# Optimization experiments

Measured on AMD Instinct MI355X. Metric: run time of the kernel, lower is better.

The kernel has to match this reference:

```python
import jax, jax.numpy as jnp
import numpy as np

B, M, D = 512, 96, 512
H = 8            # num_heads
DH = D // H      # head dim
NC = 3           # num_clusters
BETA = 5
MEM = 1024       # memory_size
EPS = 1e-8


def _l2norm(x, axis=-1):
    # torch F.cosine_similarity clamps each norm at eps=1e-8
    n = jnp.linalg.norm(x, axis=axis, keepdims=True)
    return x / jnp.maximum(n, EPS)


def _dynamic_clustering(sims):
    # sims: (B, M). Sort descending, split into NC equal groups,
    # per-group mean and (unbiased) std. (dynamic_clustering is not
    # defined in the source repo; this is the assumed implementation.)
    s = -jnp.sort(-sims, axis=1)               # descending
    g = s.reshape(B, NC, M // NC)
    means = g.mean(axis=-1)                    # (B, NC)
    stds = jnp.std(g, axis=-1, ddof=1)         # (B, NC)
    return means, stds


def setup_inputs() -> dict:
    key = jax.random.key(0)
    ks = jax.random.split(key, 6)
    vis_global = jax.random.normal(ks[0], (B, D), dtype=jnp.float32)
    text_features = jax.random.normal(ks[1], (B, M, D), dtype=jnp.float32)
    scale = 1.0 / np.sqrt(D)
    in_proj_w = jax.random.normal(ks[2], (3 * D, D), dtype=jnp.float32) * scale
    in_proj_b = jnp.zeros((3 * D,), dtype=jnp.float32)
    out_proj_w = jax.random.normal(ks[3], (D, D), dtype=jnp.float32) * scale
    out_proj_b = jnp.zeros((D,), dtype=jnp.float32)
    text_memory = jax.random.normal(ks[4], (MEM, D), dtype=jnp.float32)
    tau_p_log = jnp.log(jnp.asarray(0.1, dtype=jnp.float32))
    tau_n_log = jnp.log(jnp.asarray(0.05, dtype=jnp.float32))
    return dict(vis_global=vis_global, text_features=text_features,
                in_proj_w=in_proj_w, in_proj_b=in_proj_b,
                out_proj_w=out_proj_w, out_proj_b=out_proj_b,
                text_memory=text_memory, tau_p_log=tau_p_log, tau_n_log=tau_n_log)


def reference(vis_global, text_features, in_proj_w, in_proj_b,
              out_proj_w, out_proj_b, text_memory, tau_p_log, tau_n_log):
    # --- dynamic clustering over visual-text cosine sims ---
    sims = jnp.einsum('bd,bmd->bm', _l2norm(vis_global), _l2norm(text_features))
    means, stds = _dynamic_clustering(sims)
    cluster_scores = means / (stds + 1e-6)     # (B, NC)

    # --- MultiheadAttention: 1-token query, M-token key/value ---
    wq, wk, wv = in_proj_w[:D], in_proj_w[D:2 * D], in_proj_w[2 * D:]
    bq, bk, bv = in_proj_b[:D], in_proj_b[D:2 * D], in_proj_b[2 * D:]
    q = (vis_global @ wq.T + bq).reshape(B, H, DH)              # (B,H,DH)
    k = (text_features @ wk.T + bk).reshape(B, M, H, DH)        # (B,M,H,DH)
    v = (text_features @ wv.T + bv).reshape(B, M, H, DH)
    attn = jax.nn.softmax(jnp.einsum('bhd,bmhd->bhm', q, k) / np.sqrt(DH), axis=-1)
    ctx = jnp.einsum('bhm,bmhd->bhd', attn, v).reshape(B, D)
    corrected = ctx @ out_proj_w.T + out_proj_b                 # (B, D)

    tau_p = jnp.exp(tau_p_log)
    tau_n = jnp.exp(tau_n_log)
    pos_sim = jnp.sum(_l2norm(vis_global) * _l2norm(corrected), axis=-1)  # (B,)

    # memory-bank scatter (ptr starts at 0) + negatives, all detached
    corr_sg = jax.lax.stop_gradient(corrected)
    mem = text_memory.at[0:B].set(corr_sg)
    all_negs = jnp.concatenate([jnp.roll(corr_sg, 1, axis=0), mem], axis=0)  # (B+MEM, D)

    neg_sims = _l2norm(vis_global) @ _l2norm(all_negs).T        # (B, B+MEM)
    hard_negs, _ = jax.lax.top_k(neg_sims, BETA)                # (B, BETA)

    pos_term = jnp.exp(pos_sim / tau_p)
    neg_terms = jnp.exp(hard_negs / tau_n).sum(axis=1)
    loss = -jnp.mean(jnp.log(pos_term / (pos_term + neg_terms + 1e-8)))
    return loss, corrected, cluster_scores
```

## Files before the change

### kernel.cpp

```cpp
#include <hip/hip_runtime.h>
#include <math.h>

typedef unsigned short u16;
typedef unsigned int u32;
typedef __attribute__((ext_vector_type(8))) short short8;
typedef __attribute__((ext_vector_type(4))) float f32x4;

#define EPS 1e-8f

__device__ inline float bf2f(u16 u) {
    union { u32 i; float f; } v; v.i = ((u32)u) << 16; return v.f;
}
__device__ inline u16 f2bf(float f) {
    union { float f; u32 u; } v; v.f = f;
    u32 r = v.u + 0x7fffu + ((v.u >> 16) & 1u);
    return (u16)(r >> 16);
}
__device__ inline u32 pack2(float a, float b) {
    return (u32)f2bf(a) | ((u32)f2bf(b) << 16);
}
__device__ inline float wave_sum(float v) {
    for (int off = 32; off; off >>= 1) v += __shfl_xor(v, off, 64);
    return v;
}

__global__ __launch_bounds__(256) void prep(const float* __restrict__ vis,
                                            const float* __restrict__ ipw,
                                            const float* __restrict__ opw,
                                            float* __restrict__ vis_n,
                                            u16* __restrict__ vis_nb,
                                            u16* __restrict__ vis_b,
                                            u16* __restrict__ wqb,
                                            u16* __restrict__ wvb,
                                            u16* __restrict__ wob,
                                            float* __restrict__ loss0)
{
    int bid = blockIdx.x;
    if (bid >= 128) {
        int i = ((bid - 128) * 256 + threadIdx.x) * 4;
        const float* src; u16* dst; int j;
        if (i < 262144)      { j = i;          src = ipw + j;          dst = wqb + j; }
        else if (i < 524288) { j = i - 262144; src = ipw + 524288 + j; dst = wvb + j; }
        else                 { j = i - 524288; src = opw + j;          dst = wob + j; }
        float4 v = *(const float4*)src;
        uint2 pk; pk.x = pack2(v.x, v.y); pk.y = pack2(v.z, v.w);
        *(uint2*)dst = pk;
        return;
    }
    if (bid == 0 && threadIdx.x == 0) loss0[0] = 0.0f;
    int wave = threadIdx.x >> 6, lane = threadIdx.x & 63;
    int b = bid * 4 + wave;
    const float* row = vis + b * 512 + lane * 8;
    float4 x0 = *(const float4*)row;
    float4 x1 = *(const float4*)(row + 4);
    uint4 rk;
    rk.x = pack2(x0.x, x0.y); rk.y = pack2(x0.z, x0.w);
    rk.z = pack2(x1.x, x1.y); rk.w = pack2(x1.z, x1.w);
    *(uint4*)(vis_b + b*512 + lane*8) = rk;
    float ss = x0.x*x0.x + x0.y*x0.y + x0.z*x0.z + x0.w*x0.w
             + x1.x*x1.x + x1.y*x1.y + x1.z*x1.z + x1.w*x1.w;
    ss = wave_sum(ss);
    float inv = 1.0f / fmaxf(sqrtf(ss), EPS);
    float4 y0, y1;
    y0.x = x0.x*inv; y0.y = x0.y*inv; y0.z = x0.z*inv; y0.w = x0.w*inv;
    y1.x = x1.x*inv; y1.y = x1.y*inv; y1.z = x1.z*inv; y1.w = x1.w*inv;
    *(float4*)(vis_n + b*512 + lane*8)     = y0;
    *(float4*)(vis_n + b*512 + lane*8 + 4) = y1;
    uint4 pk;
    pk.x = pack2(y0.x, y0.y); pk.y = pack2(y0.z, y0.w);
    pk.z = pack2(y1.x, y1.y); pk.w = pack2(y1.z, y1.w);
    *(uint4*)(vis_nb + b*512 + lane*8) = pk;
}

__global__ __launch_bounds__(256) void gemm64(const u16* __restrict__ A, int lda,
                                              const u16* __restrict__ B,
                                              const float* __restrict__ bias,
                                              float* __restrict__ Cf, int ldc)
{
    __shared__ __align__(16) u16 As[64 * 64];
    __shared__ __align__(16) u16 Bs[64 * 64];
    const int t = threadIdx.x, lane = t & 63, w = t >> 6;
    const int m0 = blockIdx.x * 64, n0 = blockIdx.y * 64;
    const int wm = (w >> 1) * 32, wn = (w & 1) * 32;
    const int l16 = lane & 15, quad = lane >> 4;
    const int srow = t >> 3, scol = (t & 7) * 8;

    f32x4 acc[2][2];
    for (int i = 0; i < 2; i++)
        for (int j = 0; j < 2; j++)
            for (int e = 0; e < 4; e++) acc[i][j][e] = 0.f;

    for (int ko = 0; ko < 512; ko += 64) {
        __syncthreads();
        #pragma unroll
        for (int i = 0; i < 2; i++) {
            int row = i * 32 + srow;
            *(uint4*)&As[row * 64 + scol] = *(const uint4*)&A[(size_t)(m0 + row) * lda + ko + scol];
            *(uint4*)&Bs[row * 64 + scol] = *(const uint4*)&B[(size_t)(n0 + row) * 512 + ko + scol];
        }
        __syncthreads();
        #pragma unroll
        for (int ks = 0; ks < 2; ks++) {
            short8 af[2], bfr[2];
            #pragma unroll
            for (int i = 0; i < 2; i++)
                af[i] = *(const short8*)&As[(wm + i * 16 + l16) * 64 + ks * 32 + quad * 8];
            #pragma unroll
            for (int j = 0; j < 2; j++)
                bfr[j] = *(const short8*)&Bs[(wn + j * 16 + l16) * 64 + ks * 32 + quad * 8];
            #pragma unroll
            for (int i = 0; i < 2; i++)
                #pragma unroll
                for (int j = 0; j < 2; j++)
                    acc[i][j] = __builtin_amdgcn_mfma_f32_16x16x32_bf16(af[i], bfr[j], acc[i][j], 0, 0, 0);
        }
    }
    for (int i = 0; i < 2; i++) {
        int row = m0 + wm + i * 16 + quad * 4;
        for (int j = 0; j < 2; j++) {
            int col = n0 + wn + j * 16 + l16;
            float bv = bias ? bias[col] : 0.f;
            for (int r = 0; r < 4; r++)
                Cf[(size_t)(row + r) * ldc + col] = acc[i][j][r] + bv;
        }
    }
}

__global__ __launch_bounds__(256) void gemm_head(const u16* __restrict__ u_allb,
                                                 const u16* __restrict__ wvb,
                                                 const float* __restrict__ bv,
                                                 u16* __restrict__ ctxb)
{
    const int h = blockIdx.y;
    const u16* A = u_allb + h * 512;
    const u16* B = wvb + (size_t)h * 64 * 512;
    __shared__ __align__(16) u16 As[64 * 64];
    __shared__ __align__(16) u16 Bs[64 * 64];
    const int t = threadIdx.x, lane = t & 63, w = t >> 6;
    const int m0 = blockIdx.x * 64;
    const int wm = (w >> 1) * 32, wn = (w & 1) * 32;
    const int l16 = lane & 15, quad = lane >> 4;
    const int srow = t >> 3, scol = (t & 7) * 8;

    f32x4 acc[2][2];
    for (int i = 0; i < 2; i++)
        for (int j = 0; j < 2; j++)
            for (int e = 0; e < 4; e++) acc[i][j][e] = 0.f;

    for (int ko = 0; ko < 512; ko += 64) {
        __syncthreads();
        #pragma unroll
        for (int i = 0; i < 2; i++) {
            int row = i * 32 + srow;
            *(uint4*)&As[row * 64 + scol] = *(const uint4*)&A[(size_t)(m0 + row) * 4096 + ko + scol];
            *(uint4*)&Bs[row * 64 + scol] = *(const uint4*)&B[(size_t)row * 512 + ko + scol];
        }
        __syncthreads();
        #pragma unroll
        for (int ks = 0; ks < 2; ks++) {
            short8 af[2], bfr[2];
            #pragma unroll
            for (int i = 0; i < 2; i++)
                af[i] = *(const short8*)&As[(wm + i * 16 + l16) * 64 + ks * 32 + quad * 8];
            #pragma unroll
            for (int j = 0; j < 2; j++)
                bfr[j] = *(const short8*)&Bs[(wn + j * 16 + l16) * 64 + ks * 32 + quad * 8];
            #pragma unroll
            for (int i = 0; i < 2; i++)
                #pragma unroll
                for (int j = 0; j < 2; j++)
                    acc[i][j] = __builtin_amdgcn_mfma_f32_16x16x32_bf16(af[i], bfr[j], acc[i][j], 0, 0, 0);
        }
    }
    for (int i = 0; i < 2; i++) {
        int row = m0 + wm + i * 16 + quad * 4;
        for (int j = 0; j < 2; j++) {
            int col = wn + j * 16 + l16;
            float bb = bv[h * 64 + col];
            for (int r = 0; r < 4; r++)
                ctxb[(size_t)(row + r) * 512 + h * 64 + col] = f2bf(acc[i][j][r] + bb);
        }
    }
}

__global__ __launch_bounds__(256) void qk_proj(const float* __restrict__ q,
                                               const float* __restrict__ wk,
                                               float* __restrict__ qk_all)
{
    int bg = blockIdx.x, h = blockIdx.y;
    int t = threadIdx.x;
    int j = blockIdx.z * 256 + t;
    __shared__ float q8[8][64];
    {
        int r = t >> 5;
        int d0 = (t & 31) * 2;
        const float* qp = q + (bg * 8 + r) * 512 + h * 64 + d0;
        q8[r][d0] = qp[0]; q8[r][d0 + 1] = qp[1];
    }
    __syncthreads();
    float acc[8] = {0, 0, 0, 0, 0, 0, 0, 0};
    const float* wrow = wk + (size_t)(h * 64) * 512 + j;
    #pragma unroll 4
    for (int d = 0; d < 64; d++) {
        float ww = wrow[(size_t)d * 512];
        #pragma unroll
        for (int r = 0; r < 8; r++) acc[r] += q8[r][d] * ww;
    }
    #pragma unroll
    for (int r = 0; r < 8; r++)
        qk_all[((size_t)(bg * 8 + r) * 8 + h) * 512 + j] = acc[r];
}

__global__ __launch_bounds__(1024) void fused_attn(const float* __restrict__ tf,
                                                   const float* __restrict__ vis_n,
                                                   const float* __restrict__ qk_all,
                                                   u16* __restrict__ u_allb,
                                                   float* __restrict__ out_cs)
{
    __shared__ __align__(16) u16 Xs[96 * 520];
    __shared__ __align__(16) u16 Qs[16 * 520];
    __shared__ __align__(16) u16 Ps[16 * 104];
    __shared__ float Sc[16 * 100];
    __shared__ float sm_[96], srt[96], linv[8];

    const int b = blockIdx.x;
    const int t = threadIdx.x, w = t >> 6, lane = t & 63;
    const int l16 = lane & 15, quad = lane >> 4;

    const float4* v4 = (const float4*)(vis_n + b * 512 + lane * 8);
    float4 va = v4[0], vb = v4[1];

    if (w < 8) {
        const float4* q4 = (const float4*)(qk_all + ((size_t)b * 8 + w) * 512 + lane * 8);
        float4 a = q4[0], c = q4[1];
        uint4 pk;
        pk.x = pack2(a.x, a.y); pk.y = pack2(a.z, a.w);
        pk.z = pack2(c.x, c.y); pk.w = pack2(c.z, c.w);
        *(uint4*)&Qs[w * 520 + lane * 8] = pk;
    }

    #pragma unroll
    for (int i = 0; i < 3; i++) {
        int m0r = w + i * 32;
        int m1r = m0r + 16;
        const float4* x4a = (const float4*)(tf + ((size_t)b * 96 + m0r) * 512 + lane * 8);
        const float4* x4b = (const float4*)(tf + ((size_t)b * 96 + m1r) * 512 + lane * 8);
        float4 a0 = x4a[0], c0 = x4a[1];
        float4 a1 = x4b[0], c1 = x4b[1];
        float ss0 = a0.x*a0.x + a0.y*a0.y + a0.z*a0.z + a0.w*a0.w
                  + c0.x*c0.x + c0.y*c0.y + c0.z*c0.z + c0.w*c0.w;
        float dt0 = a0.x*va.x + a0.y*va.y + a0.z*va.z + a0.w*va.w
                  + c0.x*vb.x + c0.y*vb.y + c0.z*vb.z + c0.w*vb.w;
        float ss1 = a1.x*a1.x + a1.y*a1.y + a1.z*a1.z + a1.w*a1.w
                  + c1.x*c1.x + c1.y*c1.y + c1.z*c1.z + c1.w*c1.w;
        float dt1 = a1.x*va.x + a1.y*va.y + a1.z*va.z + a1.w*va.w
                  + c1.x*vb.x + c1.y*vb.y + c1.z*vb.z + c1.w*vb.w;
        #pragma unroll
        for (int off = 32; off; off >>= 1) {
            ss0 += __shfl_xor(ss0, off, 64);
            dt0 += __shfl_xor(dt0, off, 64);
            ss1 += __shfl_xor(ss1, off, 64);
            dt1 += __shfl_xor(dt1, off, 64);
        }
        if (lane == 0) {
            sm_[m0r] = dt0 / fmaxf(sqrtf(ss0), EPS);
            sm_[m1r] = dt1 / fmaxf(sqrtf(ss1), EPS);
        }
        uint4 pk0, pk1;
        pk0.x = pack2(a0.x, a0.y); pk0.y = pack2(a0.z, a0.w);
        pk0.z = pack2(c0.x, c0.y); pk0.w = pack2(c0.z, c0.w);
        pk1.x = pack2(a1.x, a1.y); pk1.y = pack2(a1.z, a1.w);
        pk1.z = pack2(c1.x, c1.y); pk1.w = pack2(c1.z, c1.w);
        *(uint4*)&Xs[m0r * 520 + lane * 8] = pk0;
        *(uint4*)&Xs[m1r * 520 + lane * 8] = pk1;
    }
    __syncthreads();

    if (w < 6) {
        f32x4 acc;
        for (int e = 0; e < 4; e++) acc[e] = 0.f;
        #pragma unroll
        for (int ks = 0; ks < 16; ks++) {
            short8 a = *(const short8*)&Xs[(w * 16 + l16) * 520 + ks * 32 + quad * 8];
            short8 q = *(const short8*)&Qs[l16 * 520 + ks * 32 + quad * 8];
            acc = __builtin_amdgcn_mfma_f32_16x16x32_bf16(a, q, acc, 0, 0, 0);
        }
        #pragma unroll
        for (int r = 0; r < 4; r++)
            Sc[l16 * 100 + w * 16 + quad * 4 + r] = acc[r] * 0.125f;
    }
    __syncthreads();

    if (w < 8) {
        float e0 = __expf(Sc[w * 100 + lane]);
        float e1 = (lane < 32) ? __expf(Sc[w * 100 + 64 + lane]) : 0.f;
        float l = wave_sum(e0 + e1);
        Ps[w * 104 + lane] = f2bf(e0);
        if (lane < 32) Ps[w * 104 + 64 + lane] = f2bf(e1);
        if (lane == 0) linv[w] = 1.0f / l;
    }
    if (t < 96) {
        float v = sm_[t]; int r = 0;
        for (int j = 0; j < 96; j++) {
            float u = sm_[j];
            r += (u > v) || (u == v && j < t);
        }
        srt[r] = v;
    }
    __syncthreads();

    #pragma unroll
    for (int jj = 0; jj < 2; jj++) {
        int n0 = (w * 2 + jj) * 16;
        f32x4 acc;
        for (int e = 0; e < 4; e++) acc[e] = 0.f;
        #pragma unroll
        for (int ks = 0; ks < 3; ks++) {
            short8 ap = *(const short8*)&Ps[l16 * 104 + ks * 32 + quad * 8];
            short8 bx;
            #pragma unroll
            for (int j = 0; j < 8; j++)
                bx[j] = (short)Xs[(ks * 32 + quad * 8 + j) * 520 + n0 + l16];
            acc = __builtin_amdgcn_mfma_f32_16x16x32_bf16(ap, bx, acc, 0, 0, 0);
        }
        if (quad < 2) {
            #pragma unroll
            for (int r = 0; r < 4; r++) {
                int h = quad * 4 + r;
                u_allb[((size_t)b * 8 + h) * 512 + n0 + l16] = f2bf(acc[r] * linv[h]);
            }
        }
    }
    if (t < 3) {
        float mean = 0.f;
        #pragma unroll 8
        for (int i = 0; i < 32; i++) mean += srt[t * 32 + i];
        mean *= (1.0f / 32.0f);
        float var = 0.f;
        #pragma unroll 8
        for (int i = 0; i < 32; i++) { float d = srt[t * 32 + i] - mean; var += d * d; }
        var *= (1.0f / 31.0f);
        out_cs[b * 3 + t] = mean / (sqrtf(var) + 1e-6f);
    }
}

__global__ __launch_bounds__(256) void negs_build(const float* __restrict__ corrected,
                                                  const float* __restrict__ tm,
                                                  const float* __restrict__ vis_n,
                                                  u16* __restrict__ negs_nb,
                                                  float* __restrict__ pos)
{
    int wave = threadIdx.x >> 6, lane = threadIdx.x & 63;
    int j = blockIdx.x * 4 + wave;
    const float* src = (j < 512) ? (corrected + j * 512) : (tm + j * 512);
    const float* row = src + lane * 8;
    float4 x0 = *(const float4*)row;
    float4 x1 = *(const float4*)(row + 4);
    float ss = x0.x*x0.x + x0.y*x0.y + x0.z*x0.z + x0.w*x0.w
             + x1.x*x1.x + x1.y*x1.y + x1.z*x1.z + x1.w*x1.w;
    float dt = 0.f;
    if (j < 512) {
        const float* vn = vis_n + j * 512 + lane * 8;
        float4 v0 = *(const float4*)vn;
        float4 v1 = *(const float4*)(vn + 4);
        dt = x0.x*v0.x + x0.y*v0.y + x0.z*v0.z + x0.w*v0.w
           + x1.x*v1.x + x1.y*v1.y + x1.z*v1.z + x1.w*v1.w;
    }
    ss = wave_sum(ss);
    dt = wave_sum(dt);
    float inv = 1.0f / fmaxf(sqrtf(ss), EPS);
    float4 y0, y1;
    y0.x = x0.x*inv; y0.y = x0.y*inv; y0.z = x0.z*inv; y0.w = x0.w*inv;
    y1.x = x1.x*inv; y1.y = x1.y*inv; y1.z = x1.z*inv; y1.w = x1.w*inv;
    uint4 pk;
    pk.x = pack2(y0.x, y0.y); pk.y = pack2(y0.z, y0.w);
    pk.z = pack2(y1.x, y1.y); pk.w = pack2(y1.z, y1.w);
    *(uint4*)(negs_nb + j * 512 + lane * 8) = pk;
    if (j < 512 && lane == 0) pos[j] = dt * inv;
}

__global__ __launch_bounds__(256) void topk_loss(const float* __restrict__ ns,
                                                 const float* __restrict__ pos,
                                                 const float* __restrict__ tau_p_log,
                                                 const float* __restrict__ tau_n_log,
                                                 float* __restrict__ out_loss)
{
    int b = blockIdx.x, t = threadIdx.x;
    int w = t >> 6, lane = t & 63;
    __shared__ float cand_v[4];
    __shared__ int   cand_m[4];

    const float4 raw = *(const float4*)(ns + b * 1024 + t * 4);
    float lv[4] = {raw.x, raw.y, raw.z, raw.w};
    #pragma unroll
    for (int i = 1; i < 4; i++) {
        float key = lv[i];
        int j = i - 1;
        #pragma unroll
        for (int k = 0; k < 3; k++) {
            if (j >= 0 && lv[j] < key) { lv[j + 1] = lv[j]; j--; }
        }
        lv[j + 1] = key;
    }
    int lp = 0;

    float tn = expf(tau_n_log[0]);
    float inv_tn = 1.0f / tn;
    float nsum = 0.f;
    int collected = 0;

    for (int round = 0; round < 5 && collected < 5; round++) {
        float head = (lp < 4) ? lv[lp] : -1e30f;
        float mv = head; int ml = lane;
        #pragma unroll
        for (int off = 32; off; off >>= 1) {
            float ov = __shfl_xor(mv, off, 64);
            int   ol = __shfl_xor(ml, off, 64);
            if (ov > mv || (ov == mv && ol < ml)) { mv = ov; ml = ol; }
        }
        if (lane == 0) { cand_v[w] = mv; cand_m[w] = ml; }
        __syncthreads();
        float bv = cand_v[0]; int bw = 0;
        #pragma unroll
        for (int i = 1; i < 4; i++) {
            if (cand_v[i] > bv) { bv = cand_v[i]; bw = i; }
        }
        int bl = cand_m[bw];
        __syncthreads();
        if (w == bw && lane == bl) lp++;
        int wm = ((bw * 64 + bl) < 128) ? 2 : 1;
        int take = (wm < (5 - collected)) ? wm : (5 - collected);
        nsum += (float)take * __expf(bv * inv_tn);
        collected += take;
    }

    if (t == 0) {
        float tp = expf(tau_p_log[0]);
        float p = expf(pos[b] / tp);
        float term = logf(p / (p + nsum + 1e-8f));
        atomicAdd(out_loss, -term * (1.0f / 512.0f));
    }
}

extern "C" void kernel_launch(void* const* d_in, const int* in_sizes, int n_in,
                              void* d_out, int out_size, void* d_ws, size_t ws_size,
                              hipStream_t stream) {
    const float* vis = (const float*)d_in[0];
    const float* tf  = (const float*)d_in[1];
    const float* ipw = (const float*)d_in[2];
    const float* ipb = (const float*)d_in[3];
    const float* opw = (const float*)d_in[4];
    const float* opb = (const float*)d_in[5];
    const float* tm  = (const float*)d_in[6];
    const float* tpl = (const float*)d_in[7];
    const float* tnl = (const float*)d_in[8];

    float* out       = (float*)d_out;
    float* out_loss  = out;
    float* out_corr  = out + 1;
    float* out_cs    = out + 1 + 512 * 512;

    char* p = (char*)d_ws;
    auto alloc = [&](size_t bytes) { char* r = p; p += (bytes + 255) & ~(size_t)255; return r; };
    float* vis_n  = (float*)alloc(512 * 512 * 4);
    u16*   vis_nb = (u16*)  alloc(512 * 512 * 2);
    u16*   vis_b  = (u16*)  alloc(512 * 512 * 2);
    u16*   wqb    = (u16*)  alloc(512 * 512 * 2);
    u16*   wvb    = (u16*)  alloc(512 * 512 * 2);
    u16*   wob    = (u16*)  alloc(512 * 512 * 2);
    float* qws    = (float*)alloc(512 * 512 * 4);
    float* qk_all = (float*)alloc((size_t)512 * 8 * 512 * 4);
    u16*   u_allb = (u16*)  alloc((size_t)512 * 8 * 512 * 2);
    u16*   ctxb   = (u16*)  alloc(512 * 512 * 2);
    u16*   negsb  = (u16*)  alloc(1024 * 512 * 2);
    float* ns     = (float*)alloc(512 * 1024 * 4);
    float* pos    = (float*)alloc(512 * 4);

    const float* wk = ipw + 512 * 512;
    const float* bv = ipb + 2 * 512;

    prep<<<896, 256, 0, stream>>>(vis, ipw, opw, vis_n, vis_nb, vis_b, wqb, wvb, wob, out_loss);
    gemm64<<<dim3(8, 8), 256, 0, stream>>>(vis_b, 512, wqb, ipb, qws, 512);
    qk_proj<<<dim3(64, 8, 2), 256, 0, stream>>>(qws, wk, qk_all);
    fused_attn<<<512, 1024, 0, stream>>>(tf, vis_n, qk_all, u_allb, out_cs);
    gemm_head<<<dim3(8, 8), 256, 0, stream>>>(u_allb, wvb, bv, ctxb);
    gemm64<<<dim3(8, 8), 256, 0, stream>>>(ctxb, 512, wob, opb, out_corr, 512);
    negs_build<<<256, 256, 0, stream>>>(out_corr, tm, vis_n, negsb, pos);
    gemm64<<<dim3(8, 16), 256, 0, stream>>>(vis_nb, 512, negsb, nullptr, ns, 1024);
    topk_loss<<<512, 256, 0, stream>>>(ns, pos, tpl, tnl, out_loss);
}
```

Baseline: 245.2 us.

## Fuse q/qk projections, restructure attention to two batches per block, fold negs into GEMM

Several changes land together. A new qqk kernel computes q and then q·Wk per head in one kernel, using an fp16 transposed Wk that prep builds, which replaces the separate gemm64 and qk_proj launches. fused_attn now handles two batch rows per 512-thread block and prefetches the next row's text features into registers. The negs_build kernel is removed: prep pre-normalises the memory rows, and a gemm_corr kernel writes corrected rows plus their squared norms, so normalisation is applied afterwards in topk_loss. The aim is fewer launches and less fp32 intermediate traffic, at the cost of more fp16/bf16 rounding and altered occupancy.

```diff
diff --git a/kernel.cpp b/kernel.cpp
--- a/kernel.cpp
+++ b/kernel.cpp
@@ -4,6 +4,7 @@
 typedef unsigned short u16;
 typedef unsigned int u32;
 typedef __attribute__((ext_vector_type(8))) short short8;
+typedef __attribute__((ext_vector_type(8))) _Float16 half8;
 typedef __attribute__((ext_vector_type(4))) float f32x4;
 
 #define EPS 1e-8f
@@ -16,6 +17,10 @@
     u32 r = v.u + 0x7fffu + ((v.u >> 16) & 1u);
     return (u16)(r >> 16);
 }
+__device__ inline u16 f2h(float f) {
+    _Float16 h = (_Float16)f;
+    union { _Float16 hh; u16 u; } v; v.hh = h; return v.u;
+}
 __device__ inline u32 pack2(float a, float b) {
     return (u32)f2bf(a) | ((u32)f2bf(b) << 16);
 }
@@ -27,17 +32,58 @@
 __global__ __launch_bounds__(256) void prep(const float* __restrict__ vis,
                                             const float* __restrict__ ipw,
                                             const float* __restrict__ opw,
+                                            const float* __restrict__ tm,
                                             float* __restrict__ vis_n,
                                             u16* __restrict__ vis_nb,
                                             u16* __restrict__ vis_b,
                                             u16* __restrict__ wqb,
                                             u16* __restrict__ wvb,
                                             u16* __restrict__ wob,
+                                            u16* __restrict__ negsb,
+                                            u16* __restrict__ wkT,
+                                            float* __restrict__ corrSS,
                                             float* __restrict__ loss0)
 {
     int bid = blockIdx.x;
+    int t = threadIdx.x;
+    if (bid >= 1024) {
+        __shared__ __align__(16) u16 T[64 * 72];
+        int idx = bid - 1024;
+        int a = idx >> 3, cb = idx & 7;
+        const float* wk = ipw + 262144;
+        int r = t >> 2, c0 = (t & 3) * 16;
+        #pragma unroll
+        for (int q = 0; q < 4; q++) {
+            float4 v = *(const float4*)&wk[(size_t)(a * 64 + r) * 512 + cb * 64 + c0 + q * 4];
+            T[(c0 + q * 4 + 0) * 72 + r] = f2h(v.x);
+            T[(c0 + q * 4 + 1) * 72 + r] = f2h(v.y);
+            T[(c0 + q * 4 + 2) * 72 + r] = f2h(v.z);
+            T[(c0 + q * 4 + 3) * 72 + r] = f2h(v.w);
+        }
+        __syncthreads();
+        int j = t >> 2, ch = (t & 3) * 16;
+        *(uint4*)&wkT[(size_t)(cb * 64 + j) * 512 + a * 64 + ch]     = *(const uint4*)&T[j * 72 + ch];
+        *(uint4*)&wkT[(size_t)(cb * 64 + j) * 512 + a * 64 + ch + 8] = *(const uint4*)&T[j * 72 + ch + 8];
+        return;
+    }
+    if (bid >= 896) {
+        int wave = t >> 6, lane = t & 63;
+        int j = 512 + (bid - 896) * 4 + wave;
+        const float* row = tm + (size_t)j * 512 + lane * 8;
+        float4 x0 = *(const float4*)row;
+        float4 x1 = *(const float4*)(row + 4);
+        float ss = x0.x*x0.x + x0.y*x0.y + x0.z*x0.z + x0.w*x0.w
+                 + x1.x*x1.x + x1.y*x1.y + x1.z*x1.z + x1.w*x1.w;
+        ss = wave_sum(ss);
+        float inv = 1.0f / fmaxf(sqrtf(ss), EPS);
+        uint4 pk;
+        pk.x = pack2(x0.x*inv, x0.y*inv); pk.y = pack2(x0.z*inv, x0.w*inv);
+        pk.z = pack2(x1.x*inv, x1.y*inv); pk.w = pack2(x1.z*inv, x1.w*inv);
+        *(uint4*)(negsb + (size_t)j * 512 + lane * 8) = pk;
+        return;
+    }
     if (bid >= 128) {
-        int i = ((bid - 128) * 256 + threadIdx.x) * 4;
+        int i = ((bid - 128) * 256 + t) * 4;
         const float* src; u16* dst; int j;
         if (i < 262144)      { j = i;          src = ipw + j;          dst = wqb + j; }
         else if (i < 524288) { j = i - 262144; src = ipw + 524288 + j; dst = wvb + j; }
@@ -47,16 +93,20 @@
         *(uint2*)dst = pk;
         return;
     }
-    if (bid == 0 && threadIdx.x == 0) loss0[0] = 0.0f;
-    int wave = threadIdx.x >> 6, lane = threadIdx.x & 63;
+    if (bid == 0) {
+        if (t == 0) loss0[0] = 0.0f;
+        corrSS[t] = 0.0f;
+        corrSS[t + 256] = 0.0f;
+    }
+    int wave = t >> 6, lane = t & 63;
     int b = bid * 4 + wave;
-    const float* row = vis + b * 512 + lane * 8;
+    const float* row = vis + (size_t)b * 512 + lane * 8;
     float4 x0 = *(const float4*)row;
     float4 x1 = *(const float4*)(row + 4);
     uint4 rk;
     rk.x = pack2(x0.x, x0.y); rk.y = pack2(x0.z, x0.w);
     rk.z = pack2(x1.x, x1.y); rk.w = pack2(x1.z, x1.w);
-    *(uint4*)(vis_b + b*512 + lane*8) = rk;
+    *(uint4*)(vis_b + (size_t)b * 512 + lane * 8) = rk;
     float ss = x0.x*x0.x + x0.y*x0.y + x0.z*x0.z + x0.w*x0.w
              + x1.x*x1.x + x1.y*x1.y + x1.z*x1.z + x1.w*x1.w;
     ss = wave_sum(ss);
@@ -64,23 +114,25 @@
     float4 y0, y1;
     y0.x = x0.x*inv; y0.y = x0.y*inv; y0.z = x0.z*inv; y0.w = x0.w*inv;
     y1.x = x1.x*inv; y1.y = x1.y*inv; y1.z = x1.z*inv; y1.w = x1.w*inv;
-    *(float4*)(vis_n + b*512 + lane*8)     = y0;
-    *(float4*)(vis_n + b*512 + lane*8 + 4) = y1;
+    *(float4*)(vis_n + (size_t)b * 512 + lane * 8)     = y0;
+    *(float4*)(vis_n + (size_t)b * 512 + lane * 8 + 4) = y1;
     uint4 pk;
     pk.x = pack2(y0.x, y0.y); pk.y = pack2(y0.z, y0.w);
     pk.z = pack2(y1.x, y1.y); pk.w = pack2(y1.z, y1.w);
-    *(uint4*)(vis_nb + b*512 + lane*8) = pk;
-}
-
-__global__ __launch_bounds__(256) void gemm64(const u16* __restrict__ A, int lda,
-                                              const u16* __restrict__ B,
-                                              const float* __restrict__ bias,
-                                              float* __restrict__ Cf, int ldc)
+    *(uint4*)(vis_nb + (size_t)b * 512 + lane * 8) = pk;
+}
+
+__global__ __launch_bounds__(256) void qqk(const u16* __restrict__ visb,
+                                           const u16* __restrict__ wqb,
+                                           const float* __restrict__ ipb,
+                                           const u16* __restrict__ wkT,
+                                           u16* __restrict__ qkb)
 {
-    __shared__ __align__(16) u16 As[64 * 64];
-    __shared__ __align__(16) u16 Bs[64 * 64];
+    __shared__ __align__(16) u16 As[64 * 72];
+    __shared__ __align__(16) u16 Bs[64 * 72];
+    __shared__ __align__(16) u16 Qf[64 * 72];
     const int t = threadIdx.x, lane = t & 63, w = t >> 6;
-    const int m0 = blockIdx.x * 64, n0 = blockIdx.y * 64;
+    const int m0 = blockIdx.x * 64, h = blockIdx.y;
     const int wm = (w >> 1) * 32, wn = (w & 1) * 32;
     const int l16 = lane & 15, quad = lane >> 4;
     const int srow = t >> 3, scol = (t & 7) * 8;
@@ -95,8 +147,8 @@
         #pragma unroll
         for (int i = 0; i < 2; i++) {
             int row = i * 32 + srow;
-            *(uint4*)&As[row * 64 + scol] = *(const uint4*)&A[(size_t)(m0 + row) * lda + ko + scol];
-            *(uint4*)&Bs[row * 64 + scol] = *(const uint4*)&B[(size_t)(n0 + row) * 512 + ko + scol];
+            *(uint4*)&As[row * 72 + scol] = *(const uint4*)&visb[(size_t)(m0 + row) * 512 + ko + scol];
+            *(uint4*)&Bs[row * 72 + scol] = *(const uint4*)&wqb[(size_t)(h * 64 + row) * 512 + ko + scol];
         }
         __syncthreads();
         #pragma unroll
@@ -104,10 +156,10 @@
             short8 af[2], bfr[2];
             #pragma unroll
             for (int i = 0; i < 2; i++)
-                af[i] = *(const short8*)&As[(wm + i * 16 + l16) * 64 + ks * 32 + quad * 8];
+                af[i] = *(const short8*)&As[(wm + i * 16 + l16) * 72 + ks * 32 + quad * 8];
             #pragma unroll
             for (int j = 0; j < 2; j++)
-                bfr[j] = *(const short8*)&Bs[(wn + j * 16 + l16) * 64 + ks * 32 + quad * 8];
+                bfr[j] = *(const short8*)&Bs[(wn + j * 16 + l16) * 72 + ks * 32 + quad * 8];
             #pragma unroll
             for (int i = 0; i < 2; i++)
                 #pragma unroll
@@ -115,14 +167,195 @@
                     acc[i][j] = __builtin_amdgcn_mfma_f32_16x16x32_bf16(af[i], bfr[j], acc[i][j], 0, 0, 0);
         }
     }
-    for (int i = 0; i < 2; i++) {
-        int row = m0 + wm + i * 16 + quad * 4;
-        for (int j = 0; j < 2; j++) {
-            int col = n0 + wn + j * 16 + l16;
-            float bv = bias ? bias[col] : 0.f;
+    #pragma unroll
+    for (int i = 0; i < 2; i++)
+        #pragma unroll
+        for (int j = 0; j < 2; j++)
+            #pragma unroll
+            for (int r = 0; r < 4; r++) {
+                int rl = wm + i * 16 + quad * 4 + r;
+                int cl = wn + j * 16 + l16;
+                Qf[rl * 72 + cl] = f2h(acc[i][j][r] + ipb[h * 64 + cl]);
+            }
+    for (int jt = 0; jt < 8; jt++) {
+        __syncthreads();
+        #pragma unroll
+        for (int i = 0; i < 2; i++) {
+            int row = i * 32 + srow;
+            *(uint4*)&Bs[row * 72 + scol] = *(const uint4*)&wkT[(size_t)(jt * 64 + row) * 512 + h * 64 + scol];
+        }
+        __syncthreads();
+        f32x4 a2[2][2];
+        for (int i = 0; i < 2; i++)
+            for (int j = 0; j < 2; j++)
+                for (int e = 0; e < 4; e++) a2[i][j][e] = 0.f;
+        #pragma unroll
+        for (int ks = 0; ks < 2; ks++) {
+            half8 af[2], bfr[2];
+            #pragma unroll
+            for (int i = 0; i < 2; i++)
+                af[i] = *(const half8*)&Qf[(wm + i * 16 + l16) * 72 + ks * 32 + quad * 8];
+            #pragma unroll
+            for (int j = 0; j < 2; j++)
+                bfr[j] = *(const half8*)&Bs[(wn + j * 16 + l16) * 72 + ks * 32 + quad * 8];
+            #pragma unroll
+            for (int i = 0; i < 2; i++)
+                #pragma unroll
+                for (int j = 0; j < 2; j++)
+                    a2[i][j] = __builtin_amdgcn_mfma_f32_16x16x32_f16(af[i], bfr[j], a2[i][j], 0, 0, 0);
+        }
+        #pragma unroll
+        for (int i = 0; i < 2; i++)
+            #pragma unroll
+            for (int j = 0; j < 2; j++)
+                #pragma unroll
+                for (int r = 0; r < 4; r++) {
+                    int rb = m0 + wm + i * 16 + quad * 4 + r;
+                    int cj = jt * 64 + wn + j * 16 + l16;
+                    qkb[((size_t)rb * 8 + h) * 512 + cj] = f2bf(a2[i][j][r]);
+                }
+    }
+}
+
+__global__ __launch_bounds__(512) void fused_attn(const float* __restrict__ tf,
+                                                  const float* __restrict__ vis_n,
+                                                  const u16* __restrict__ qkb,
+                                                  u16* __restrict__ u_allb,
+                                                  float* __restrict__ out_cs)
+{
+    __shared__ __align__(16) u16 Xs[96 * 520];
+    __shared__ __align__(16) u16 Qs[16 * 520];
+    __shared__ __align__(16) u16 Ps[16 * 104];
+    __shared__ float Sc[16 * 100];
+    __shared__ float sm_[96], srt[96], linv[8];
+
+    const int b0 = blockIdx.x * 2;
+    const int t = threadIdx.x, w = t >> 6, lane = t & 63;
+    const int l16 = lane & 15, quad = lane >> 4;
+
+    float4 xr[12][2];
+    #pragma unroll
+    for (int i = 0; i < 6; i++) {
+        int m0r = w + i * 16, m1r = m0r + 8;
+        const float4* pa = (const float4*)(tf + ((size_t)b0 * 96 + m0r) * 512 + lane * 8);
+        const float4* pb = (const float4*)(tf + ((size_t)b0 * 96 + m1r) * 512 + lane * 8);
+        xr[2*i][0]   = pa[0]; xr[2*i][1]   = pa[1];
+        xr[2*i+1][0] = pb[0]; xr[2*i+1][1] = pb[1];
+    }
+
+    for (int ib = 0; ib < 2; ib++) {
+        const int b = b0 + ib;
+        const float4* v4 = (const float4*)(vis_n + (size_t)b * 512 + lane * 8);
+        float4 va = v4[0], vb = v4[1];
+
+        #pragma unroll
+        for (int i = 0; i < 6; i++) {
+            int m0r = w + i * 16, m1r = m0r + 8;
+            float4 a0 = xr[2*i][0],   c0 = xr[2*i][1];
+            float4 a1 = xr[2*i+1][0], c1 = xr[2*i+1][1];
+            if (ib == 0) {
+                const float4* pa = (const float4*)(tf + ((size_t)(b0 + 1) * 96 + m0r) * 512 + lane * 8);
+                const float4* pb = (const float4*)(tf + ((size_t)(b0 + 1) * 96 + m1r) * 512 + lane * 8);
+                xr[2*i][0]   = pa[0]; xr[2*i][1]   = pa[1];
+                xr[2*i+1][0] = pb[0]; xr[2*i+1][1] = pb[1];
+            }
+            float ss0 = a0.x*a0.x + a0.y*a0.y + a0.z*a0.z + a0.w*a0.w
+                      + c0.x*c0.x + c0.y*c0.y + c0.z*c0.z + c0.w*c0.w;
+            float dt0 = a0.x*va.x + a0.y*va.y + a0.z*va.z + a0.w*va.w
+                      + c0.x*vb.x + c0.y*vb.y + c0.z*vb.z + c0.w*vb.w;
+            float ss1 = a1.x*a1.x + a1.y*a1.y + a1.z*a1.z + a1.w*a1.w
+                      + c1.x*c1.x + c1.y*c1.y + c1.z*c1.z + c1.w*c1.w;
+            float dt1 = a1.x*va.x + a1.y*va.y + a1.z*va.z + a1.w*va.w
+                      + c1.x*vb.x + c1.y*vb.y + c1.z*vb.z + c1.w*vb.w;
+            #pragma unroll
+            for (int off = 32; off; off >>= 1) {
+                ss0 += __shfl_xor(ss0, off, 64);
+                dt0 += __shfl_xor(dt0, off, 64);
+                ss1 += __shfl_xor(ss1, off, 64);
+                dt1 += __shfl_xor(dt1, off, 64);
+            }
+            if (lane == 0) {
+                sm_[m0r] = dt0 / fmaxf(sqrtf(ss0), EPS);
+                sm_[m1r] = dt1 / fmaxf(sqrtf(ss1), EPS);
+            }
+            uint4 pk0, pk1;
+            pk0.x = pack2(a0.x, a0.y); pk0.y = pack2(a0.z, a0.w);
+            pk0.z = pack2(c0.x, c0.y); pk0.w = pack2(c0.z, c0.w);
+            pk1.x = pack2(a1.x, a1.y); pk1.y = pack2(a1.z, a1.w);
+            pk1.z = pack2(c1.x, c1.y); pk1.w = pack2(c1.z, c1.w);
+            *(uint4*)&Xs[m0r * 520 + lane * 8] = pk0;
+            *(uint4*)&Xs[m1r * 520 + lane * 8] = pk1;
+        }
+        *(uint4*)&Qs[w * 520 + lane * 8] = *(const uint4*)(qkb + ((size_t)b * 8 + w) * 512 + lane * 8);
+        __syncthreads();
+
+        if (w < 6) {
+            f32x4 acc;
+            for (int e = 0; e < 4; e++) acc[e] = 0.f;
+            #pragma unroll
+            for (int ks = 0; ks < 16; ks++) {
+                short8 a = *(const short8*)&Xs[(w * 16 + l16) * 520 + ks * 32 + quad * 8];
+                short8 q = *(const short8*)&Qs[l16 * 520 + ks * 32 + quad * 8];
+                acc = __builtin_amdgcn_mfma_f32_16x16x32_bf16(a, q, acc, 0, 0, 0);
+            }
+            #pragma unroll
             for (int r = 0; r < 4; r++)
-                Cf[(size_t)(row + r) * ldc + col] = acc[i][j][r] + bv;
-        }
+                Sc[l16 * 100 + w * 16 + quad * 4 + r] = acc[r] * 0.125f;
+        }
+        __syncthreads();
+
+        {
+            float e0 = __expf(Sc[w * 100 + lane]);
+            float e1 = (lane < 32) ? __expf(Sc[w * 100 + 64 + lane]) : 0.f;
+            float l = wave_sum(e0 + e1);
+            Ps[w * 104 + lane] = f2bf(e0);
+            if (lane < 32) Ps[w * 104 + 64 + lane] = f2bf(e1);
+            if (lane == 0) linv[w] = 1.0f / l;
+        }
+        if (t < 96) {
+            float v = sm_[t]; int r = 0;
+            for (int j = 0; j < 96; j++) {
+                float u = sm_[j];
+                r += (u > v) || (u == v && j < t);
+            }
+            srt[r] = v;
+        }
+        __syncthreads();
+
+        #pragma unroll
+        for (int jj = 0; jj < 4; jj++) {
+            int n0 = (w * 4 + jj) * 16;
+            f32x4 acc;
+            for (int e = 0; e < 4; e++) acc[e] = 0.f;
+            #pragma unroll
+            for (int ks = 0; ks < 3; ks++) {
+                short8 ap = *(const short8*)&Ps[l16 * 104 + ks * 32 + quad * 8];
+                short8 bx;
+                #pragma unroll
+                for (int j = 0; j < 8; j++)
+                    bx[j] = (short)Xs[(ks * 32 + quad * 8 + j) * 520 + n0 + l16];
+                acc = __builtin_amdgcn_mfma_f32_16x16x32_bf16(ap, bx, acc, 0, 0, 0);
+            }
+            if (quad < 2) {
+                #pragma unroll
+                for (int r = 0; r < 4; r++) {
+                    int h = quad * 4 + r;
+                    u_allb[((size_t)b * 8 + h) * 512 + n0 + l16] = f2bf(acc[r] * linv[h]);
+                }
+            }
+        }
+        if (t < 3) {
+            float mean = 0.f;
+            #pragma unroll 8
+            for (int i = 0; i < 32; i++) mean += srt[t * 32 + i];
+            mean *= (1.0f / 32.0f);
+            float var = 0.f;
+            #pragma unroll 8
+            for (int i = 0; i < 32; i++) { float d = srt[t * 32 + i] - mean; var += d * d; }
+            var *= (1.0f / 31.0f);
+            out_cs[b * 3 + t] = mean / (sqrtf(var) + 1e-6f);
+        }
+        __syncthreads();
     }
 }
 
@@ -134,8 +367,8 @@
     const int h = blockIdx.y;
     const u16* A = u_allb + h * 512;
     const u16* B = wvb + (size_t)h * 64 * 512;
-    __shared__ __align__(16) u16 As[64 * 64];
-    __shared__ __align__(16) u16 Bs[64 * 64];
+    __shared__ __align__(16) u16 As[64 * 72];
+    __shared__ __align__(16) u16 Bs[64 * 72];
     const int t = threadIdx.x, lane = t & 63, w = t >> 6;
     const int m0 = blockIdx.x * 64;
     const int wm = (w >> 1) * 32, wn = (w & 1) * 32;
@@ -152,8 +385,8 @@
         #pragma unroll
         for (int i = 0; i < 2; i++) {
             int row = i * 32 + srow;
-            *(uint4*)&As[row * 64 + scol] = *(const uint4*)&A[(size_t)(m0 + row) * 4096 + ko + scol];
-            *(uint4*)&Bs[row * 64 + scol] = *(const uint4*)&B[(size_t)row * 512 + ko + scol];
+            *(uint4*)&As[row * 72 + scol] = *(const uint4*)&A[(size_t)(m0 + row) * 4096 + ko + scol];
+            *(uint4*)&Bs[row * 72 + scol] = *(const uint4*)&B[(size_t)row * 512 + ko + scol];
         }
         __syncthreads();
         #pragma unroll
@@ -161,10 +394,10 @@
             short8 af[2], bfr[2];
             #pragma unroll
             for (int i = 0; i < 2; i++)
-                af[i] = *(const short8*)&As[(wm + i * 16 + l16) * 64 + ks * 32 + quad * 8];
+                af[i] = *(const short8*)&As[(wm + i * 16 + l16) * 72 + ks * 32 + quad * 8];
             #pragma unroll
             for (int j = 0; j < 2; j++)
-                bfr[j] = *(const short8*)&Bs[(wn + j * 16 + l16) * 64 + ks * 32 + quad * 8];
+                bfr[j] = *(const short8*)&Bs[(wn + j * 16 + l16) * 72 + ks * 32 + quad * 8];
             #pragma unroll
             for (int i = 0; i < 2; i++)
                 #pragma unroll
@@ -183,262 +416,210 @@
     }
 }
 
-__global__ __launch_bounds__(256) void qk_proj(const float* __restrict__ q,
-                                               const float* __restrict__ wk,
-                                               float* __restrict__ qk_all)
+__global__ __launch_bounds__(256) void gemm_corr(const u16* __restrict__ A,
+                                                 const u16* __restrict__ B,
+                                                 const float* __restrict__ bias,
+                                                 float* __restrict__ Cf,
+                                                 u16* __restrict__ corrB,
+                                                 float* __restrict__ corrSS)
 {
-    int bg = blockIdx.x, h = blockIdx.y;
-    int t = threadIdx.x;
-    int j = blockIdx.z * 256 + t;
-    __shared__ float q8[8][64];
-    {
-        int r = t >> 5;
-        int d0 = (t & 31) * 2;
-        const float* qp = q + (bg * 8 + r) * 512 + h * 64 + d0;
-        q8[r][d0] = qp[0]; q8[r][d0 + 1] = qp[1];
-    }
-    __syncthreads();
-    float acc[8] = {0, 0, 0, 0, 0, 0, 0, 0};
-    const float* wrow = wk + (size_t)(h * 64) * 512 + j;
-    #pragma unroll 4
-    for (int d = 0; d < 64; d++) {
-        float ww = wrow[(size_t)d * 512];
-        #pragma unroll
-        for (int r = 0; r < 8; r++) acc[r] += q8[r][d] * ww;
+    __shared__ __align__(16) u16 As[64 * 72];
+    __shared__ __align__(16) u16 Bs[64 * 72];
+    const int t = threadIdx.x, lane = t & 63, w = t >> 6;
+    const int m0 = blockIdx.x * 64, n0 = blockIdx.y * 64;
+    const int wm = (w >> 1) * 32, wn = (w & 1) * 32;
+    const int l16 = lane & 15, quad = lane >> 4;
+    const int srow = t >> 3, scol = (t & 7) * 8;
+
+    f32x4 acc[2][2];
+    for (int i = 0; i < 2; i++)
+        for (int j = 0; j < 2; j++)
+            for (int e = 0; e < 4; e++) acc[i][j][e] = 0.f;
+
+    for (int ko = 0; ko < 512; ko += 64) {
+        __syncthreads();
+        #pragma unroll
+        for (int i = 0; i < 2; i++) {
+            int row = i * 32 + srow;
+            *(uint4*)&As[row * 72 + scol] = *(const uint4*)&A[(size_t)(m0 + row) * 512 + ko + scol];
+            *(uint4*)&Bs[row * 72 + scol] = *(const uint4*)&B[(size_t)(n0 + row) * 512 + ko + scol];
+        }
+        __syncthreads();
+        #pragma unroll
+        for (int ks = 0; ks < 2; ks++) {
+            short8 af[2], bfr[2];
+            #pragma unroll
+            for (int i = 0; i < 2; i++)
+                af[i] = *(const short8*)&As[(wm + i * 16 + l16) * 72 + ks * 32 + quad * 8];
+            #pragma unroll
+            for (int j = 0; j < 2; j++)
+                bfr[j] = *(const short8*)&Bs[(wn + j * 16 + l16) * 72 + ks * 32 + quad * 8];
+            #pragma unroll
+            for (int i = 0; i < 2; i++)
+                #pragma unroll
+                for (int j = 0; j < 2; j++)
+                    acc[i][j] = __builtin_amdgcn_mfma_f32_16x16x32_bf16(af[i], bfr[j], acc[i][j], 0, 0, 0);
+        }
     }
     #pragma unroll
-    for (int r = 0; r < 8; r++)
-        qk_all[((size_t)(bg * 8 + r) * 8 + h) * 512 + j] = acc[r];
-}
-
-__global__ __launch_bounds__(1024) void fused_attn(const float* __restrict__ tf,
-                                                   const float* __restrict__ vis_n,
-                                                   const float* __restrict__ qk_all,
-                                                   u16* __restrict__ u_allb,
-                                                   float* __restrict__ out_cs)
+    for (int i = 0; i < 2; i++) {
+        #pragma unroll
+        for (int r = 0; r < 4; r++) {
+            int row = m0 + wm + i * 16 + quad * 4 + r;
+            float s = 0.f;
+            #pragma unroll
+            for (int j = 0; j < 2; j++) {
+                int col = n0 + wn + j * 16 + l16;
+                float v = acc[i][j][r] + bias[col];
+                Cf[(size_t)row * 512 + col] = v;
+                corrB[(size_t)row * 512 + col] = f2bf(v);
+                s += v * v;
+            }
+            s += __shfl_xor(s, 1, 64); s += __shfl_xor(s, 2, 64);
+            s += __shfl_xor(s, 4, 64); s += __shfl_xor(s, 8, 64);
+            if (l16 == 0) atomicAdd(&corrSS[row], s);
+        }
+    }
+}
+
+__global__ __launch_bounds__(256) void gemm64(const u16* __restrict__ A, int lda,
+                                              const u16* __restrict__ B,
+                                              const float* __restrict__ bias,
+                                              float* __restrict__ Cf, int ldc)
 {
-    __shared__ __align__(16) u16 Xs[96 * 520];
-    __shared__ __align__(16) u16 Qs[16 * 520];
-    __shared__ __align__(16) u16 Ps[16 * 104];
-    __shared__ float Sc[16 * 100];
-    __shared__ float sm_[96], srt[96], linv[8];
-
-    const int b = blockIdx.x;
-    const int t = threadIdx.x, w = t >> 6, lane = t & 63;
+    __shared__ __align__(16) u16 As[64 * 72];
+    __shared__ __align__(16) u16 Bs[64 * 72];
+    const int t = threadIdx.x, lane = t & 63, w = t >> 6;
+    const int m0 = blockIdx.x * 64, n0 = blockIdx.y * 64;
+    const int wm = (w >> 1) * 32, wn = (w & 1) * 32;
     const int l16 = lane & 15, quad = lane >> 4;
-
-    const float4* v4 = (const float4*)(vis_n + b * 512 + lane * 8);
-    float4 va = v4[0], vb = v4[1];
-
-    if (w < 8) {
-        const float4* q4 = (const float4*)(qk_all + ((size_t)b * 8 + w) * 512 + lane * 8);
-        float4 a = q4[0], c = q4[1];
-        uint4 pk;
-        pk.x = pack2(a.x, a.y); pk.y = pack2(a.z, a.w);
-        pk.z = pack2(c.x, c.y); pk.w = pack2(c.z, c.w);
-        *(uint4*)&Qs[w * 520 + lane * 8] = pk;
-    }
-
-    #pragma unroll
-    for (int i = 0; i < 3; i++) {
-        int m0r = w + i * 32;
-        int m1r = m0r + 16;
-        const float4* x4a = (const float4*)(tf + ((size_t)b * 96 + m0r) * 512 + lane * 8);
-        const float4* x4b = (const float4*)(tf + ((size_t)b * 96 + m1r) * 512 + lane * 8);
-        float4 a0 = x4a[0], c0 = x4a[1];
-        float4 a1 = x4b[0], c1 = x4b[1];
-        float ss0 = a0.x*a0.x + a0.y*a0.y + a0.z*a0.z + a0.w*a0.w
-                  + c0.x*c0.x + c0.y*c0.y + c0.z*c0.z + c0.w*c0.w;
-        float dt0 = a0.x*va.x + a0.y*va.y + a0.z*va.z + a0.w*va.w
-                  + c0.x*vb.x + c0.y*vb.y + c0.z*vb.z + c0.w*vb.w;
-        float ss1 = a1.x*a1.x + a1.y*a1.y + a1.z*a1.z + a1.w*a1.w
-                  + c1.x*c1.x + c1.y*c1.y + c1.z*c1.z + c1.w*c1.w;
-        float dt1 = a1.x*va.x + a1.y*va.y + a1.z*va.z + a1.w*va.w
-                  + c1.x*vb.x + c1.y*vb.y + c1.z*vb.z + c1.w*vb.w;
-        #pragma unroll
-        for (int off = 32; off; off >>= 1) {
-            ss0 += __shfl_xor(ss0, off, 64);
-            dt0 += __shfl_xor(dt0, off, 64);
-            ss1 += __shfl_xor(ss1, off, 64);
-            dt1 += __shfl_xor(dt1, off, 64);
-        }
-        if (lane == 0) {
-            sm_[m0r] = dt0 / fmaxf(sqrtf(ss0), EPS);
-            sm_[m1r] = dt1 / fmaxf(sqrtf(ss1), EPS);
-        }
-        uint4 pk0, pk1;
-        pk0.x = pack2(a0.x, a0.y); pk0.y = pack2(a0.z, a0.w);
-        pk0.z = pack2(c0.x, c0.y); pk0.w = pack2(c0.z, c0.w);
-        pk1.x = pack2(a1.x, a1.y); pk1.y = pack2(a1.z, a1.w);
-        pk1.z = pack2(c1.x, c1.y); pk1.w = pack2(c1.z, c1.w);
-        *(uint4*)&Xs[m0r * 520 + lane * 8] = pk0;
-        *(uint4*)&Xs[m1r * 520 + lane * 8] = pk1;
-    }
-    __syncthreads();
-
-    if (w < 6) {
-        f32x4 acc;
-        for (int e = 0; e < 4; e++) acc[e] = 0.f;
-        #pragma unroll
-        for (int ks = 0; ks < 16; ks++) {
-            short8 a = *(const short8*)&Xs[(w * 16 + l16) * 520 + ks * 32 + quad * 8];
-            short8 q = *(const short8*)&Qs[l16 * 520 + ks * 32 + quad * 8];
-            acc = __builtin_amdgcn_mfma_f32_16x16x32_bf16(a, q, acc, 0, 0, 0);
-        }
-        #pragma unroll
-        for (int r = 0; r < 4; r++)
-            Sc[l16 * 100 + w * 16 + quad * 4 + r] = acc[r] * 0.125f;
-    }
-    __syncthreads();
-
-    if (w < 8) {
-        float e0 = __expf(Sc[w * 100 + lane]);
-        float e1 = (lane < 32) ? __expf(Sc[w * 100 + 64 + lane]) : 0.f;
-        float l = wave_sum(e0 + e1);
-        Ps[w * 104 + lane] = f2bf(e0);
-        if (lane < 32) Ps[w * 104 + 64 + lane] = f2bf(e1);
-        if (lane == 0) linv[w] = 1.0f / l;
-    }
-    if (t < 96) {
-        float v = sm_[t]; int r = 0;
-        for (int j = 0; j < 96; j++) {
-            float u = sm_[j];
-            r += (u > v) || (u == v && j < t);
-        }
-        srt[r] = v;
-    }
-    __syncthreads();
-
-    #pragma unroll
-    for (int jj = 0; jj < 2; jj++) {
-        int n0 = (w * 2 + jj) * 16;
-        f32x4 acc;
-        for (int e = 0; e < 4; e++) acc[e] = 0.f;
-        #pragma unroll
-        for (int ks = 0; ks < 3; ks++) {
-            short8 ap = *(const short8*)&Ps[l16 * 104 + ks * 32 + quad * 8];
-            short8 bx;
-            #pragma unroll
-            for (int j = 0; j < 8; j++)
-                bx[j] = (short)Xs[(ks * 32 + quad * 8 + j) * 520 + n0 + l16];
-            acc = __builtin_amdgcn_mfma_f32_16x16x32_bf16(ap, bx, acc, 0, 0, 0);
-        }
-        if (quad < 2) {
-            #pragma unroll
-            for (int r = 0; r < 4; r++) {
-                int h = quad * 4 + r;
-                u_allb[((size_t)b * 8 + h) * 512 + n0 + l16] = f2bf(acc[r] * linv[h]);
-            }
-        }
-    }
-    if (t < 3) {
-        float mean = 0.f;
-        #pragma unroll 8
-        for (int i = 0; i < 32; i++) mean += srt[t * 32 + i];
-        mean *= (1.0f / 32.0f);
-        float var = 0.f;
-        #pragma unroll 8
-        for (int i = 0; i < 32; i++) { float d = srt[t * 32 + i] - mean; var += d * d; }
-        var *= (1.0f / 31.0f);
-        out_cs[b * 3 + t] = mean / (sqrtf(var) + 1e-6f);
-    }
-}
-
-__global__ __launch_bounds__(256) void negs_build(const float* __restrict__ corrected,
-                                                  const float* __restrict__ tm,
-                                                  const float* __restrict__ vis_n,
-                                                  u16* __restrict__ negs_nb,
-                                                  float* __restrict__ pos)
-{
-    int wave = threadIdx.x >> 6, lane = threadIdx.x & 63;
-    int j = blockIdx.x * 4 + wave;
-    const float* src = (j < 512) ? (corrected + j * 512) : (tm + j * 512);
-    const float* row = src + lane * 8;
-    float4 x0 = *(const float4*)row;
-    float4 x1 = *(const float4*)(row + 4);
-    float ss = x0.x*x0.x + x0.y*x0.y + x0.z*x0.z + x0.w*x0.w
-             + x1.x*x1.x + x1.y*x1.y + x1.z*x1.z + x1.w*x1.w;
-    float dt = 0.f;
-    if (j < 512) {
-        const float* vn = vis_n + j * 512 + lane * 8;
-        float4 v0 = *(const float4*)vn;
-        float4 v1 = *(const float4*)(vn + 4);
-        dt = x0.x*v0.x + x0.y*v0.y + x0.z*v0.z + x0.w*v0.w
-           + x1.x*v1.x + x1.y*v1.y + x1.z*v1.z + x1.w*v1.w;
-    }
-    ss = wave_sum(ss);
-    dt = wave_sum(dt);
-    float inv = 1.0f / fmaxf(sqrtf(ss), EPS);
-    float4 y0, y1;
-    y0.x = x0.x*inv; y0.y = x0.y*inv; y0.z = x0.z*inv; y0.w = x0.w*inv;
-    y1.x = x1.x*inv; y1.y = x1.y*inv; y1.z = x1.z*inv; y1.w = x1.w*inv;
-    uint4 pk;
-    pk.x = pack2(y0.x, y0.y); pk.y = pack2(y0.z, y0.w);
-    pk.z = pack2(y1.x, y1.y); pk.w = pack2(y1.z, y1.w);
-    *(uint4*)(negs_nb + j * 512 + lane * 8) = pk;
-    if (j < 512 && lane == 0) pos[j] = dt * inv;
+    const int srow = t >> 3, scol = (t & 7) * 8;
+
+    f32x4 acc[2][2];
+    for (int i = 0; i < 2; i++)
+        for (int j = 0; j < 2; j++)
+            for (int e = 0; e < 4; e++) acc[i][j][e] = 0.f;
+
+    for (int ko = 0; ko < 512; ko += 64) {
+        __syncthreads();
+        #pragma unroll
+        for (int i = 0; i < 2; i++) {
+            int row = i * 32 + srow;
+            *(uint4*)&As[row * 72 + scol] = *(const uint4*)&A[(size_t)(m0 + row) * lda + ko + scol];
+            *(uint4*)&Bs[row * 72 + scol] = *(const uint4*)&B[(size_t)(n0 + row) * 512 + ko + scol];
+        }
+        __syncthreads();
+        #pragma unroll
+        for (int ks = 0; ks < 2; ks++) {
+            short8 af[2], bfr[2];
+            #pragma unroll
+            for (int i = 0; i < 2; i++)
+                af[i] = *(const short8*)&As[(wm + i * 16 + l16) * 72 + ks * 32 + quad * 8];
+            #pragma unroll
+            for (int j = 0; j < 2; j++)
+                bfr[j] = *(const short8*)&Bs[(wn + j * 16 + l16) * 72 + ks * 32 + quad * 8];
+            #pragma unroll
+            for (int i = 0; i < 2; i++)
+                #pragma unroll
+                for (int j = 0; j < 2; j++)
+                    acc[i][j] = __builtin_amdgcn_mfma_f32_16x16x32_bf16(af[i], bfr[j], acc[i][j], 0, 0, 0);
+        }
+    }
+    for (int i = 0; i < 2; i++) {
+        int row = m0 + wm + i * 16 + quad * 4;
+        for (int j = 0; j < 2; j++) {
+            int col = n0 + wn + j * 16 + l16;
+            float bvv = bias ? bias[col] : 0.f;
+            for (int r = 0; r < 4; r++)
+                Cf[(size_t)(row + r) * ldc + col] = acc[i][j][r] + bvv;
+        }
+    }
 }
 
 __global__ __launch_bounds__(256) void topk_loss(const float* __restrict__ ns,
-                                                 const float* __restrict__ pos,
+                                                 const float* __restrict__ corrSS,
                                                  const float* __restrict__ tau_p_log,
                                                  const float* __restrict__ tau_n_log,
                                                  float* __restrict__ out_loss)
 {
+    __shared__ float invn[512];
+    __shared__ float cv[20];
+    __shared__ int   cjx[20];
     int b = blockIdx.x, t = threadIdx.x;
     int w = t >> 6, lane = t & 63;
-    __shared__ float cand_v[4];
-    __shared__ int   cand_m[4];
-
-    const float4 raw = *(const float4*)(ns + b * 1024 + t * 4);
+
+    {
+        float s0 = corrSS[t], s1 = corrSS[t + 256];
+        invn[t]       = 1.0f / fmaxf(sqrtf(s0), EPS);
+        invn[t + 256] = 1.0f / fmaxf(sqrtf(s1), EPS);
+    }
+    __syncthreads();
+
+    const float4 raw = *(const float4*)(ns + (size_t)b * 1024 + t * 4);
     float lv[4] = {raw.x, raw.y, raw.z, raw.w};
+    int   li[4] = {t * 4, t * 4 + 1, t * 4 + 2, t * 4 + 3};
+    if (t < 128) {
+        lv[0] *= invn[t * 4];     lv[1] *= invn[t * 4 + 1];
+        lv[2] *= invn[t * 4 + 2]; lv[3] *= invn[t * 4 + 3];
+    }
     #pragma unroll
     for (int i = 1; i < 4; i++) {
-        float key = lv[i];
+        float kv = lv[i]; int kx = li[i];
         int j = i - 1;
         #pragma unroll
         for (int k = 0; k < 3; k++) {
-            if (j >= 0 && lv[j] < key) { lv[j + 1] = lv[j]; j--; }
-        }
-        lv[j + 1] = key;
+            if (j >= 0 && lv[j] < kv) { lv[j + 1] = lv[j]; li[j + 1] = li[j]; j--; }
+        }
+        lv[j + 1] = kv; li[j + 1] = kx;
     }
     int lp = 0;
-
-    float tn = expf(tau_n_log[0]);
-    float inv_tn = 1.0f / tn;
-    float nsum = 0.f;
-    int collected = 0;
-
-    for (int round = 0; round < 5 && collected < 5; round++) {
-        float head = (lp < 4) ? lv[lp] : -1e30f;
-        float mv = head; int ml = lane;
+    #pragma unroll
+    for (int rd = 0; rd < 5; rd++) {
+        float mv = (lp < 4) ? lv[lp] : -1e30f;
+        int   mi = (lp < 4) ? li[lp] : 0;
+        int   ml = lane;
         #pragma unroll
         for (int off = 32; off; off >>= 1) {
             float ov = __shfl_xor(mv, off, 64);
+            int   oi = __shfl_xor(mi, off, 64);
             int   ol = __shfl_xor(ml, off, 64);
-            if (ov > mv || (ov == mv && ol < ml)) { mv = ov; ml = ol; }
-        }
-        if (lane == 0) { cand_v[w] = mv; cand_m[w] = ml; }
-        __syncthreads();
-        float bv = cand_v[0]; int bw = 0;
-        #pragma unroll
-        for (int i = 1; i < 4; i++) {
-            if (cand_v[i] > bv) { bv = cand_v[i]; bw = i; }
-        }
-        int bl = cand_m[bw];
-        __syncthreads();
-        if (w == bw && lane == bl) lp++;
-        int wm = ((bw * 64 + bl) < 128) ? 2 : 1;
-        int take = (wm < (5 - collected)) ? wm : (5 - collected);
-        nsum += (float)take * __expf(bv * inv_tn);
-        collected += take;
-    }
-
-    if (t == 0) {
-        float tp = expf(tau_p_log[0]);
-        float p = expf(pos[b] / tp);
-        float term = logf(p / (p + nsum + 1e-8f));
-        atomicAdd(out_loss, -term * (1.0f / 512.0f));
+            if (ov > mv || (ov == mv && ol < ml)) { mv = ov; mi = oi; ml = ol; }
+        }
+        if (lane == ml) lp++;
+        if (lane == 0) { cv[w * 5 + rd] = mv; cjx[w * 5 + rd] = mi; }
+    }
+    __syncthreads();
+    if (w == 0) {
+        float v  = (lane < 20) ? cv[lane] : -1e30f;
+        int   jx = (lane < 20) ? cjx[lane] : 0;
+        float tn = expf(tau_n_log[0]);
+        float itn = 1.0f / tn;
+        float nsum = 0.f; int coll = 0;
+        #pragma unroll
+        for (int rd = 0; rd < 5; rd++) {
+            float mv = v; int ml = lane; int mj = jx;
+            #pragma unroll
+            for (int off = 32; off; off >>= 1) {
+                float ov = __shfl_xor(mv, off, 64);
+                int   oj = __shfl_xor(mj, off, 64);
+                int   ol = __shfl_xor(ml, off, 64);
+                if (ov > mv || (ov == mv && ol < ml)) { mv = ov; mj = oj; ml = ol; }
+            }
+            int mult = (mj < 512) ? 2 : 1;
+            int take = 5 - coll;
+            take = (mult < take) ? mult : take;
+            if (take < 0) take = 0;
+            nsum += (float)take * __expf(mv * itn);
+            coll += take;
+            if (lane == ml) v = -1e30f;
+        }
+        if (lane == 0) {
+            float pos = ns[(size_t)b * 1024 + b] * invn[b];
+            float tp = expf(tau_p_log[0]);
+            float p = expf(pos / tp);
+            float term = logf(p / (p + nsum + 1e-8f));
+            atomicAdd(out_loss, -term * (1.0f / 512.0f));
+        }
     }
 }
 
@@ -468,24 +649,22 @@
     u16*   wqb    = (u16*)  alloc(512 * 512 * 2);
     u16*   wvb    = (u16*)  alloc(512 * 512 * 2);
     u16*   wob    = (u16*)  alloc(512 * 512 * 2);
-    float* qws    = (float*)alloc(512 * 512 * 4);
-    float* qk_all = (float*)alloc((size_t)512 * 8 * 512 * 4);
+    u16*   wkT    = (u16*)  alloc(512 * 512 * 2);
+    u16*   qkb    = (u16*)  alloc((size_t)512 * 8 * 512 * 2);
     u16*   u_allb = (u16*)  alloc((size_t)512 * 8 * 512 * 2);
     u16*   ctxb   = (u16*)  alloc(512 * 512 * 2);
     u16*   negsb  = (u16*)  alloc(1024 * 512 * 2);
     float* ns     = (float*)alloc(512 * 1024 * 4);
-    float* pos    = (float*)alloc(512 * 4);
-
-    const float* wk = ipw + 512 * 512;
+    float* corrSS = (float*)alloc(512 * 4);
+
     const float* bv = ipb + 2 * 512;
 
-    prep<<<896, 256, 0, stream>>>(vis, ipw, opw, vis_n, vis_nb, vis_b, wqb, wvb, wob, out_loss);
-    gemm64<<<dim3(8, 8), 256, 0, stream>>>(vis_b, 512, wqb, ipb, qws, 512);
-    qk_proj<<<dim3(64, 8, 2), 256, 0, stream>>>(qws, wk, qk_all);
-    fused_attn<<<512, 1024, 0, stream>>>(tf, vis_n, qk_all, u_allb, out_cs);
+    prep<<<1088, 256, 0, stream>>>(vis, ipw, opw, tm, vis_n, vis_nb, vis_b,
+                                   wqb, wvb, wob, negsb, wkT, corrSS, out_loss);
+    qqk<<<dim3(8, 8), 256, 0, stream>>>(vis_b, wqb, ipb, wkT, qkb);
+    fused_attn<<<256, 512, 0, stream>>>(tf, vis_n, qkb, u_allb, out_cs);
     gemm_head<<<dim3(8, 8), 256, 0, stream>>>(u_allb, wvb, bv, ctxb);
-    gemm64<<<dim3(8, 8), 256, 0, stream>>>(ctxb, 512, wob, opb, out_corr, 512);
-    negs_build<<<256, 256, 0, stream>>>(out_corr, tm, vis_n, negsb, pos);
+    gemm_corr<<<dim3(8, 8), 256, 0, stream>>>(ctxb, wob, opb, out_corr, negsb, corrSS);
     gemm64<<<dim3(8, 16), 256, 0, stream>>>(vis_nb, 512, negsb, nullptr, ns, 1024);
-    topk_loss<<<512, 256, 0, stream>>>(ns, pos, tpl, tnl, out_loss);
-}
+    topk_loss<<<512, 256, 0, stream>>>(ns, corrSS, tpl, tnl, out_loss);
+}
```

Result: slower. 260.6 us (+6.3%).
